# Kernel optimization log

Measured on AMD Instinct MI355X. Metric: run time of the kernel, lower is better.

Reference implementation:

```python
import jax, jax.numpy as jnp
import numpy as np

PI = float(np.pi)

def setup_inputs() -> dict:
    key = jax.random.key(0)
    k1, k2 = jax.random.split(key)
    B, S, NUM_CHARS, P = 8, 8192, 95, 8
    char_idx = jax.random.randint(k1, (B, S), 0, NUM_CHARS, dtype=jnp.int32)
    positions = jnp.arange(S, dtype=jnp.int32)
    W = jax.random.normal(k2, (NUM_CHARS, P), dtype=jnp.float32)
    return {"char_idx": char_idx, "positions": positions, "W": W}

def reference(char_idx, positions, W):
    """Vectorized PhysicalTokenizer.encode (learnable Phase 2, eval mode).
    char_idx: [B,S] int, already offset by ascii_start; W: [num_chars,8].
    Returns quaternion tensor [B, S, embed_dim, 4].
    """
    embed_dim = 128
    params = W[char_idx]                                  # [B,S,8] gather
    omega = params[..., 0:1] * 2.0                        # [B,S,1]
    A1, A2, A3 = params[..., 1:2], params[..., 2:3], params[..., 3:4]
    beta = params[..., 4:5]
    gamma = jax.nn.sigmoid(params[..., 5:6])
    phi = params[..., 6:7] * PI
    j = jnp.arange(embed_dim, dtype=jnp.float32)          # [D]
    # spectral wave synthesis, fused elementwise over [B,S,D]
    wave = (A1 * jnp.sin(omega * j + phi)
            + A2 * jnp.sin(2.0 * omega * j + 2.0 * phi)
            + A3 * jnp.sin(3.0 * omega * j + 3.0 * phi)) * jnp.exp(-gamma * j)
    pos_phase = jnp.sin(positions.astype(jnp.float32) * (0.1 * PI))  # [S]
    wave = wave + beta * j * pos_phase[None, :, None]     # [B,S,D]
    psi0 = wave
    psi1 = jnp.roll(wave, shift=1, axis=-1)
    psi2 = jnp.sin(wave)
    psi3 = jnp.cos(wave)
    return jnp.stack([psi0, psi1, psi2, psi3], axis=-1)   # [B,S,D,4]
```

## Files before the change

### kernel.cpp

```cpp
#include <hip/hip_runtime.h>

#define PI_F 3.14159265358979323846f

constexpr int ED = 128;
constexpr int ROWS_PER_BLOCK = 4;

__global__ __launch_bounds__(256) void ptok_kernel(
    const int* __restrict__ char_idx,
    const int* __restrict__ positions,
    const float* __restrict__ W,
    float* __restrict__ out,
    int S)
{
    const int lane = threadIdx.x & 63;
    const int wv = threadIdx.x >> 6;
    const int row = blockIdx.x * ROWS_PER_BLOCK + wv;
    const int s = row & (S - 1);

    const int c = char_idx[row];
    const float4 p0 = reinterpret_cast<const float4*>(W + c * 8)[0];
    const float4 p1 = reinterpret_cast<const float4*>(W + c * 8)[1];
    const float omega = p0.x * 2.0f;
    const float A1 = p0.y, A2 = p0.z, A3 = p0.w;
    const float beta = p1.x;
    const float gamma = 1.0f / (1.0f + __expf(-p1.y));
    const float phi = p1.z * PI_F;

    const float pos_phase = __sinf((float)positions[s] * (0.1f * PI_F));

    float w01[2];
    #pragma unroll
    for (int k = 0; k < 2; ++k) {
        const float fj = (float)(lane + 64 * k);
        const float a = omega * fj + phi;
        const float sa = __sinf(a);
        const float ca = __cosf(a);
        const float wave = (A1 * sa + A2 * (2.0f * sa * ca)
                            + A3 * sa * (3.0f - 4.0f * sa * sa))
                           * __expf(-gamma * fj);
        w01[k] = wave + beta * fj * pos_phase;
    }

    const int lm1 = (lane + 63) & 63;
    const float u0 = __shfl(w01[0], lm1, 64);
    const float u1 = __shfl(w01[1], lm1, 64);
    const float prev0 = (lane == 0) ? u1 : u0;
    const float prev1 = (lane == 0) ? u0 : u1;

    float4* orow = reinterpret_cast<float4*>(out) + (size_t)row * ED;
    float4 o0, o1;
    o0.x = w01[0]; o0.y = prev0; o0.z = __sinf(w01[0]); o0.w = __cosf(w01[0]);
    o1.x = w01[1]; o1.y = prev1; o1.z = __sinf(w01[1]); o1.w = __cosf(w01[1]);
    orow[lane] = o0;
    orow[64 + lane] = o1;
}

extern "C" void kernel_launch(void* const* d_in, const int* in_sizes, int n_in,
                              void* d_out, int out_size, void* d_ws, size_t ws_size,
                              hipStream_t stream) {
    const int* char_idx  = (const int*)d_in[0];
    const int* positions = (const int*)d_in[1];
    const float* W       = (const float*)d_in[2];
    float* out = (float*)d_out;

    const int nrows = in_sizes[0];
    const int S = in_sizes[1];

    const int grid = nrows / ROWS_PER_BLOCK;
    ptok_kernel<<<grid, 256, 0, stream>>>(char_idx, positions, W, out, S);
}
```

Baseline: 26.40 us.

## Precompute per-character wave table and position phases in a prologue kernel

Adds a small kernel that evaluates the per-character spectral wave base and the beta*j factor for all 95x128 entries, plus the per-position sine phase, and stores them in workspace. The main kernel then does one table lookup and an FMA per element instead of the sin/cos/exp synthesis. The aim is to remove transcendental work from the output-bandwidth-bound main kernel, at the cost of an extra kernel launch and a dependent table read. The table is rebuilt on every call, so no results are reused across calls.

```diff
diff --git a/kernel.cpp b/kernel.cpp
--- a/kernel.cpp
+++ b/kernel.cpp
@@ -3,12 +3,44 @@
 #define PI_F 3.14159265358979323846f
 
 constexpr int ED = 128;
+constexpr int NCHARS = 95;
 constexpr int ROWS_PER_BLOCK = 4;
 
-__global__ __launch_bounds__(256) void ptok_kernel(
-    const int* __restrict__ char_idx,
+constexpr size_t PP_OFF = 98304;
+
+__global__ __launch_bounds__(256) void build_tables(
     const int* __restrict__ positions,
     const float* __restrict__ W,
+    float2* __restrict__ tbl,
+    float* __restrict__ pp,
+    int S)
+{
+    const int i = blockIdx.x * 256 + threadIdx.x;
+    if (i < NCHARS * ED) {
+        const int c = i >> 7;
+        const int j = i & (ED - 1);
+        const float* p = W + c * 8;
+        const float omega = p[0] * 2.0f;
+        const float A1 = p[1], A2 = p[2], A3 = p[3];
+        const float beta = p[4];
+        const float gamma = 1.0f / (1.0f + expf(-p[5]));
+        const float phi = p[6] * PI_F;
+        const float fj = (float)j;
+        const float base = (A1 * sinf(omega * fj + phi)
+                          + A2 * sinf(2.0f * omega * fj + 2.0f * phi)
+                          + A3 * sinf(3.0f * omega * fj + 3.0f * phi))
+                         * expf(-gamma * fj);
+        tbl[i] = make_float2(base, beta * fj);
+    }
+    if (i < S) {
+        pp[i] = sinf((float)positions[i] * (0.1f * PI_F));
+    }
+}
+
+__global__ __launch_bounds__(256) void ptok_main(
+    const int* __restrict__ char_idx,
+    const float2* __restrict__ tbl,
+    const float* __restrict__ pp,
     float* __restrict__ out,
     int S)
 {
@@ -18,39 +50,23 @@
     const int s = row & (S - 1);
 
     const int c = char_idx[row];
-    const float4 p0 = reinterpret_cast<const float4*>(W + c * 8)[0];
-    const float4 p1 = reinterpret_cast<const float4*>(W + c * 8)[1];
-    const float omega = p0.x * 2.0f;
-    const float A1 = p0.y, A2 = p0.z, A3 = p0.w;
-    const float beta = p1.x;
-    const float gamma = 1.0f / (1.0f + __expf(-p1.y));
-    const float phi = p1.z * PI_F;
+    const float pp_s = pp[s];
 
-    const float pos_phase = __sinf((float)positions[s] * (0.1f * PI_F));
-
-    float w01[2];
-    #pragma unroll
-    for (int k = 0; k < 2; ++k) {
-        const float fj = (float)(lane + 64 * k);
-        const float a = omega * fj + phi;
-        const float sa = __sinf(a);
-        const float ca = __cosf(a);
-        const float wave = (A1 * sa + A2 * (2.0f * sa * ca)
-                            + A3 * sa * (3.0f - 4.0f * sa * sa))
-                           * __expf(-gamma * fj);
-        w01[k] = wave + beta * fj * pos_phase;
-    }
+    const float2 t0 = tbl[c * ED + lane];
+    const float2 t1 = tbl[c * ED + 64 + lane];
+    const float w0 = fmaf(t0.y, pp_s, t0.x);
+    const float w1 = fmaf(t1.y, pp_s, t1.x);
 
     const int lm1 = (lane + 63) & 63;
-    const float u0 = __shfl(w01[0], lm1, 64);
-    const float u1 = __shfl(w01[1], lm1, 64);
+    const float u0 = __shfl(w0, lm1, 64);
+    const float u1 = __shfl(w1, lm1, 64);
     const float prev0 = (lane == 0) ? u1 : u0;
     const float prev1 = (lane == 0) ? u0 : u1;
 
     float4* orow = reinterpret_cast<float4*>(out) + (size_t)row * ED;
     float4 o0, o1;
-    o0.x = w01[0]; o0.y = prev0; o0.z = __sinf(w01[0]); o0.w = __cosf(w01[0]);
-    o1.x = w01[1]; o1.y = prev1; o1.z = __sinf(w01[1]); o1.w = __cosf(w01[1]);
+    o0.x = w0; o0.y = prev0; o0.z = __sinf(w0); o0.w = __cosf(w0);
+    o1.x = w1; o1.y = prev1; o1.z = __sinf(w1); o1.w = __cosf(w1);
     orow[lane] = o0;
     orow[64 + lane] = o1;
 }
@@ -66,6 +82,13 @@
     const int nrows = in_sizes[0];
     const int S = in_sizes[1];
 
-    const int grid = nrows / ROWS_PER_BLOCK;
-    ptok_kernel<<<grid, 256, 0, stream>>>(char_idx, positions, W, out, S);
+    float2* tbl = (float2*)d_ws;
+    float* pp = (float*)((char*)d_ws + PP_OFF);
+
+    const int build_threads = (NCHARS * ED > S) ? NCHARS * ED : S;
+    build_tables<<<(build_threads + 255) / 256, 256, 0, stream>>>(
+        positions, W, tbl, pp, S);
+
+    ptok_main<<<nrows / ROWS_PER_BLOCK, 256, 0, stream>>>(
+        char_idx, tbl, pp, out, S);
 }
```

Result: slower. 31.11 us (+17.8%).

## Precompute per-character, per-phase psi table and gather-copy rows into output

Applied to the files above, without the earlier changes.

Uses the fact that sin(pos*0.1*pi) repeats every 20 integer positions, so each output row depends only on the pair (char, pos mod 20). A first kernel builds a 95x20x128 float4 table in workspace, and a second kernel copies the selected table row into the output with nontemporal stores. This removes the per-row transcendental math, at the cost of an extra launch and about 3.9MB of table reads. The original fused kernel is kept as a fallback when the workspace is too small.

```diff
diff --git a/kernel.cpp b/kernel.cpp
--- a/kernel.cpp
+++ b/kernel.cpp
@@ -3,30 +3,29 @@
 #define PI_F 3.14159265358979323846f
 
 constexpr int ED = 128;
-constexpr int ROWS_PER_BLOCK = 4;
+constexpr int NPH = 20;
+constexpr int NCHARS = 95;
+constexpr int NCOMBO = NCHARS * NPH;
 
-__global__ __launch_bounds__(256) void ptok_kernel(
-    const int* __restrict__ char_idx,
-    const int* __restrict__ positions,
+typedef float f4 __attribute__((ext_vector_type(4)));
+
+__global__ __launch_bounds__(256) void build_psi(
     const float* __restrict__ W,
-    float* __restrict__ out,
-    int S)
+    float4* __restrict__ tbl)
 {
     const int lane = threadIdx.x & 63;
     const int wv = threadIdx.x >> 6;
-    const int row = blockIdx.x * ROWS_PER_BLOCK + wv;
-    const int s = row & (S - 1);
+    const int combo = blockIdx.x * 4 + wv;
+    const int c = combo / NPH;
+    const int ph = combo - c * NPH;
 
-    const int c = char_idx[row];
-    const float4 p0 = reinterpret_cast<const float4*>(W + c * 8)[0];
-    const float4 p1 = reinterpret_cast<const float4*>(W + c * 8)[1];
-    const float omega = p0.x * 2.0f;
-    const float A1 = p0.y, A2 = p0.z, A3 = p0.w;
-    const float beta = p1.x;
-    const float gamma = 1.0f / (1.0f + __expf(-p1.y));
-    const float phi = p1.z * PI_F;
-
-    const float pos_phase = __sinf((float)positions[s] * (0.1f * PI_F));
+    const float* p = W + c * 8;
+    const float omega = p[0] * 2.0f;
+    const float A1 = p[1], A2 = p[2], A3 = p[3];
+    const float beta = p[4];
+    const float gamma = 1.0f / (1.0f + __expf(-p[5]));
+    const float phi = p[6] * PI_F;
+    const float pos_phase = __sinf((float)ph * (0.1f * PI_F));
 
     float w01[2];
     #pragma unroll
@@ -47,6 +46,77 @@
     const float prev0 = (lane == 0) ? u1 : u0;
     const float prev1 = (lane == 0) ? u0 : u1;
 
+    const float4 o0 = make_float4(w01[0], prev0, __sinf(w01[0]), __cosf(w01[0]));
+    const float4 o1 = make_float4(w01[1], prev1, __sinf(w01[1]), __cosf(w01[1]));
+    tbl[(size_t)combo * ED + lane] = o0;
+    tbl[(size_t)combo * ED + 64 + lane] = o1;
+}
+
+__global__ __launch_bounds__(256) void ptok_copy(
+    const int* __restrict__ char_idx,
+    const int* __restrict__ positions,
+    const f4* __restrict__ tbl,
+    f4* __restrict__ out,
+    int S)
+{
+    const int lane = threadIdx.x & 63;
+    const int wv = threadIdx.x >> 6;
+    const int row = blockIdx.x * 4 + wv;
+    const int s = row & (S - 1);
+
+    const int c = char_idx[row];
+    int ph = positions[s] % NPH;
+    if (ph < 0) ph += NPH;
+
+    const f4* trow = tbl + ((c * NPH + ph) << 7);
+    f4* orow = out + ((size_t)row << 7);
+
+    const f4 a = trow[lane];
+    const f4 b = trow[64 + lane];
+    __builtin_nontemporal_store(a, orow + lane);
+    __builtin_nontemporal_store(b, orow + 64 + lane);
+}
+
+__global__ __launch_bounds__(256) void ptok_fused(
+    const int* __restrict__ char_idx,
+    const int* __restrict__ positions,
+    const float* __restrict__ W,
+    float* __restrict__ out,
+    int S)
+{
+    const int lane = threadIdx.x & 63;
+    const int wv = threadIdx.x >> 6;
+    const int row = blockIdx.x * 4 + wv;
+    const int s = row & (S - 1);
+
+    const int c = char_idx[row];
+    const float4 p0 = reinterpret_cast<const float4*>(W + c * 8)[0];
+    const float4 p1 = reinterpret_cast<const float4*>(W + c * 8)[1];
+    const float omega = p0.x * 2.0f;
+    const float A1 = p0.y, A2 = p0.z, A3 = p0.w;
+    const float beta = p1.x;
+    const float gamma = 1.0f / (1.0f + __expf(-p1.y));
+    const float phi = p1.z * PI_F;
+    const float pos_phase = __sinf((float)positions[s] * (0.1f * PI_F));
+
+    float w01[2];
+    #pragma unroll
+    for (int k = 0; k < 2; ++k) {
+        const float fj = (float)(lane + 64 * k);
+        const float a = omega * fj + phi;
+        const float sa = __sinf(a);
+        const float ca = __cosf(a);
+        const float wave = (A1 * sa + A2 * (2.0f * sa * ca)
+                            + A3 * sa * (3.0f - 4.0f * sa * sa))
+                           * __expf(-gamma * fj);
+        w01[k] = wave + beta * fj * pos_phase;
+    }
+    const int lm1 = (lane + 63) & 63;
+    const float u0 = __shfl(w01[0], lm1, 64);
+    const float u1 = __shfl(w01[1], lm1, 64);
+    const float prev0 = (lane == 0) ? u1 : u0;
+    const float prev1 = (lane == 0) ? u0 : u1;
+
     float4* orow = reinterpret_cast<float4*>(out) + (size_t)row * ED;
     float4 o0, o1;
     o0.x = w01[0]; o0.y = prev0; o0.z = __sinf(w01[0]); o0.w = __cosf(w01[0]);
@@ -61,11 +131,18 @@
     const int* char_idx  = (const int*)d_in[0];
     const int* positions = (const int*)d_in[1];
     const float* W       = (const float*)d_in[2];
-    float* out = (float*)d_out;
 
     const int nrows = in_sizes[0];
     const int S = in_sizes[1];
 
-    const int grid = nrows / ROWS_PER_BLOCK;
-    ptok_kernel<<<grid, 256, 0, stream>>>(char_idx, positions, W, out, S);
+    const size_t TBL_BYTES = (size_t)NCOMBO * ED * sizeof(float4);
+
+    if (ws_size >= TBL_BYTES) {
+        build_psi<<<NCOMBO / 4, 256, 0, stream>>>(W, (float4*)d_ws);
+        ptok_copy<<<nrows / 4, 256, 0, stream>>>(
+            char_idx, positions, (const f4*)d_ws, (f4*)d_out, S);
+    } else {
+        ptok_fused<<<nrows / 4, 256, 0, stream>>>(
+            char_idx, positions, W, (float*)d_out, S);
+    }
 }
```

Measured after the change: 35.86 us. +35.9%, slower.

## Precompute per-character constants in a setup kernel and derive upper-half sines algebraically

Applied to the files above, without the earlier changes.

A small setup kernel writes a per-character constant table into the workspace: omega, phi, scaled amplitudes, sigmoid gamma, and sin/cos/exp for a shift of 64. It also writes a 20-entry position-phase table, since sin(p·0.1π) repeats every 20 integer positions. The main kernel reads these constants through a wave-uniform index. It gets the second half of each row (j+64) from the first half by angle addition and an envelope multiply, so fewer transcendental calls are needed per thread. The cost is an extra kernel launch and a workspace dependency, with a fallback to the old fused kernel. Since the kernel is dominated by output stores, the compute saved may be small.

```diff
diff --git a/kernel.cpp b/kernel.cpp
--- a/kernel.cpp
+++ b/kernel.cpp
@@ -3,9 +3,99 @@
 #define PI_F 3.14159265358979323846f
 
 constexpr int ED = 128;
-constexpr int ROWS_PER_BLOCK = 4;
+constexpr int NCHARS = 95;
+constexpr int RPB = 4;
+constexpr int TSTRIDE = 16;
+constexpr int PP_OFF = NCHARS * TSTRIDE + 16;
 
-__global__ __launch_bounds__(256) void ptok_kernel(
+typedef float f4 __attribute__((ext_vector_type(4)));
+
+__global__ __launch_bounds__(128) void build_consts(
+    const float* __restrict__ W, float* __restrict__ ws)
+{
+    const int t = threadIdx.x;
+    if (t < NCHARS) {
+        const float* p = W + t * 8;
+        const float omega = p[0] * 2.0f;
+        const float g = 1.0f / (1.0f + expf(-p[5]));
+        float* T = ws + t * TSTRIDE;
+        T[0] = omega;
+        T[1] = p[6] * PI_F;
+        T[2] = p[1];
+        T[3] = 2.0f * p[2];
+        T[4] = p[3];
+        T[5] = p[4];
+        T[6] = g;
+        T[7] = sinf(64.0f * omega);
+        T[8] = cosf(64.0f * omega);
+        T[9] = expf(-64.0f * g);
+        T[10] = 0.0f; T[11] = 0.0f; T[12] = 0.0f;
+        T[13] = 0.0f; T[14] = 0.0f; T[15] = 0.0f;
+    } else if (t >= 96 && t < 96 + 20) {
+        ws[PP_OFF + (t - 96)] = sinf((float)(t - 96) * (0.1f * PI_F));
+    }
+}
+
+__global__ __launch_bounds__(256) void ptok_main(
+    const int* __restrict__ char_idx,
+    const int* __restrict__ positions,
+    const float* __restrict__ ws,
+    f4* __restrict__ out,
+    int S)
+{
+    const int lane = threadIdx.x & 63;
+    const int row = blockIdx.x * RPB + (threadIdx.x >> 6);
+    const int urow = __builtin_amdgcn_readfirstlane(row);
+    const int s = urow & (S - 1);
+    const int c = char_idx[urow];
+    const unsigned pv = (unsigned)positions[s];
+    const float pp = ws[PP_OFF + (pv % 20u)];
+
+    const float* T = ws + c * TSTRIDE;
+    const float omega = T[0], phi = T[1];
+    const float A1 = T[2], A2p = T[3], A3 = T[4];
+    const float bp = T[5] * pp;
+    const float g  = T[6];
+    const float s64 = T[7], c64 = T[8], e64 = T[9];
+
+    const float fj = (float)lane;
+    const float a0  = fmaf(omega, fj, phi);
+    const float sa0 = __sinf(a0);
+    const float ca0 = __cosf(a0);
+    const float env0 = __expf(-g * fj);
+    const float sa1 = fmaf(sa0, c64, ca0 * s64);
+    const float ca1 = fmaf(ca0, c64, -sa0 * s64);
+    const float env1 = env0 * e64;
+
+    const float t0 = sa0 * sa0;
+    const float s3_0 = sa0 * fmaf(-4.0f, t0, 3.0f);
+    float acc0 = A1 * sa0;
+    acc0 = fmaf(A2p, sa0 * ca0, acc0);
+    acc0 = fmaf(A3, s3_0, acc0);
+    const float w0 = fmaf(bp, fj, acc0 * env0);
+
+    const float t1 = sa1 * sa1;
+    const float s3_1 = sa1 * fmaf(-4.0f, t1, 3.0f);
+    float acc1 = A1 * sa1;
+    acc1 = fmaf(A2p, sa1 * ca1, acc1);
+    acc1 = fmaf(A3, s3_1, acc1);
+    const float w1 = fmaf(bp, fj + 64.0f, acc1 * env1);
+
+    const int lm1 = (lane + 63) & 63;
+    const float u0 = __shfl(w0, lm1, 64);
+    const float u1 = __shfl(w1, lm1, 64);
+    const float prev0 = (lane == 0) ? u1 : u0;
+    const float prev1 = (lane == 0) ? u0 : u1;
+
+    f4* orow = out + ((size_t)row << 7);
+    f4 o0, o1;
+    o0.x = w0; o0.y = prev0; o0.z = __sinf(w0); o0.w = __cosf(w0);
+    o1.x = w1; o1.y = prev1; o1.z = __sinf(w1); o1.w = __cosf(w1);
+    orow[lane] = o0;
+    orow[64 + lane] = o1;
+}
+
+__global__ __launch_bounds__(256) void ptok_fused(
     const int* __restrict__ char_idx,
     const int* __restrict__ positions,
     const float* __restrict__ W,
@@ -14,7 +104,7 @@
 {
     const int lane = threadIdx.x & 63;
     const int wv = threadIdx.x >> 6;
-    const int row = blockIdx.x * ROWS_PER_BLOCK + wv;
+    const int row = blockIdx.x * RPB + wv;
     const int s = row & (S - 1);
 
     const int c = char_idx[row];
@@ -25,7 +115,6 @@
     const float beta = p1.x;
     const float gamma = 1.0f / (1.0f + __expf(-p1.y));
     const float phi = p1.z * PI_F;
-
     const float pos_phase = __sinf((float)positions[s] * (0.1f * PI_F));
 
     float w01[2];
@@ -40,7 +129,6 @@
                            * __expf(-gamma * fj);
         w01[k] = wave + beta * fj * pos_phase;
     }
-
     const int lm1 = (lane + 63) & 63;
     const float u0 = __shfl(w01[0], lm1, 64);
     const float u1 = __shfl(w01[1], lm1, 64);
@@ -61,11 +149,18 @@
     const int* char_idx  = (const int*)d_in[0];
     const int* positions = (const int*)d_in[1];
     const float* W       = (const float*)d_in[2];
-    float* out = (float*)d_out;
 
     const int nrows = in_sizes[0];
     const int S = in_sizes[1];
 
-    const int grid = nrows / ROWS_PER_BLOCK;
-    ptok_kernel<<<grid, 256, 0, stream>>>(char_idx, positions, W, out, S);
+    const size_t NEED = (size_t)(PP_OFF + 20) * sizeof(float);
+
+    if (ws_size >= NEED) {
+        build_consts<<<1, 128, 0, stream>>>(W, (float*)d_ws);
+        ptok_main<<<nrows / RPB, 256, 0, stream>>>(
+            char_idx, positions, (const float*)d_ws, (f4*)d_out, S);
+    } else {
+        ptok_fused<<<nrows / RPB, 256, 0, stream>>>(
+            char_idx, positions, W, (float*)d_out, S);
+    }
 }
```

After: 30.45 us. +15.4%, slower.
